# Performance work log

Measured on AMD Instinct MI355X. Metric: run time of the kernel, lower is better.

## Reference

```python
import jax, jax.numpy as jnp
import numpy as np

T, H, I, E, K = 1024, 2880, 2880, 16, 4
ALPHA = 1.702   # gemm1_alpha
LIMIT = 7.0     # swiglu_limit (gemm1_clamp_limit)


def setup_inputs() -> dict:
    key = jax.random.key(0)
    ks = jax.random.split(key, 9)
    s = 0.02  # init scale to keep activations sane
    return {
        "hidden_states": jax.random.normal(ks[0], (T, H), jnp.float32),
        "router_w": jax.random.normal(ks[1], (E, H), jnp.float32) * s,
        "router_b": jax.random.normal(ks[2], (E,), jnp.float32) * s,
        "w_gate": jax.random.normal(ks[3], (E, H, I), jnp.float32) * s,
        "b_gate": jax.random.normal(ks[4], (E, I), jnp.float32) * s,
        "w_up": jax.random.normal(ks[5], (E, H, I), jnp.float32) * s,
        "b_up": jax.random.normal(ks[6], (E, I), jnp.float32) * s,
        "w_down": jax.random.normal(ks[7], (E, I, H), jnp.float32) * s,
        "b_down": jax.random.normal(ks[8], (E, H), jnp.float32) * s,
    }


def reference(hidden_states, router_w, router_b, w_gate, b_gate, w_up, b_up, w_down, b_down):
    x = hidden_states  # [T, H]
    # Router: ReplicatedLinear(hidden_size, num_experts, bias=True)
    logits = x @ router_w.T + router_b            # [T, E]
    # TopK(top_k=K, renormalize=True): softmax -> top-k -> renormalize
    probs = jax.nn.softmax(logits, axis=-1)
    top_w, top_i = jax.lax.top_k(probs, K)        # [T, K]
    top_w = top_w / jnp.sum(top_w, axis=-1, keepdims=True)
    # combine weights scattered back to [T, E] (rows sum to 1)
    comb = jnp.sum(jax.nn.one_hot(top_i, E, dtype=x.dtype) * top_w[..., None], axis=1)
    # Expert grouped GEMM (dense over experts; combine weights zero out unused)
    g = jnp.einsum('th,ehi->eti', x, w_gate) + b_gate[:, None, :]   # [E, T, I]
    u = jnp.einsum('th,ehi->eti', x, w_up) + b_up[:, None, :]       # [E, T, I]
    # gpt-oss clamped swiglu: gate clamp max, up clamp both sides
    g = jnp.minimum(g, LIMIT)
    u = jnp.clip(u, -LIMIT, LIMIT)
    act = (u + 1.0) * (g * jax.nn.sigmoid(g * ALPHA))               # [E, T, I]
    y = jnp.einsum('eti,eih->eth', act, w_down) + b_down[:, None, :]  # [E, T, H]
    out = jnp.einsum('te,eth->th', comb, y)                          # [T, H]
    return out
```

## Files before the change

### kernel.cpp

```cpp
#include <hip/hip_runtime.h>
#include <stdint.h>

#define T_TOK 1024
#define HD 2880
#define ID 2880
#define NE 16
#define NTOP 4

#define BM 128
#define BN 64
#define BK 64
#define NKT (HD / BK)
#define NIB (ID / BN)
#define NMB (T_TOK / BM)
#define NBLK (NE * NIB * NMB)

typedef short bf16x8 __attribute__((ext_vector_type(8)));
typedef float f32x4 __attribute__((ext_vector_type(4)));

__device__ __forceinline__ uint4 pack8f(const float* v) {
    union { __bf16 b[8]; uint4 q; } p;
#pragma unroll
    for (int j = 0; j < 8; j++) p.b[j] = (__bf16)v[j];
    return p.q;
}
__device__ __forceinline__ unsigned short bf16bits(float f) {
    union { __bf16 b[2]; unsigned short u[2]; } p;
    p.b[0] = (__bf16)f;
    return p.u[0];
}

__global__ __launch_bounds__(256) void k_init(float* __restrict__ out, int* __restrict__ cnt) {
    int i = blockIdx.x * 256 + threadIdx.x;
    ((float4*)out)[i] = make_float4(0.f, 0.f, 0.f, 0.f);
    if (blockIdx.x == 0 && threadIdx.x < NE) cnt[threadIdx.x] = 0;
}

__global__ __launch_bounds__(256) void k_xbf(const float* __restrict__ x, unsigned short* __restrict__ xbf) {
    const size_t i = (size_t)blockIdx.x * 256 + threadIdx.x;
    float v[8];
    float4 a = ((const float4*)x)[i * 2];
    float4 b = ((const float4*)x)[i * 2 + 1];
    v[0] = a.x; v[1] = a.y; v[2] = a.z; v[3] = a.w;
    v[4] = b.x; v[5] = b.y; v[6] = b.z; v[7] = b.w;
    ((uint4*)xbf)[i] = pack8f(v);
}

__global__ __launch_bounds__(256) void k_router(
    const float* __restrict__ x, const float* __restrict__ rw, const float* __restrict__ rb,
    float* __restrict__ topw, int* __restrict__ cnt, int* __restrict__ list)
{
    const int t = blockIdx.x;
    const int tid = threadIdx.x;
    float acc[NE];
#pragma unroll
    for (int e = 0; e < NE; e++) acc[e] = 0.f;
    for (int c = tid; c < HD; c += 256) {
        float xv = x[(size_t)t * HD + c];
#pragma unroll
        for (int e = 0; e < NE; e++) acc[e] += xv * rw[(size_t)e * HD + c];
    }
    __shared__ float red[4][NE];
    const int lane = tid & 63, wv = tid >> 6;
#pragma unroll
    for (int e = 0; e < NE; e++) {
        float v = acc[e];
#pragma unroll
        for (int off = 32; off > 0; off >>= 1) v += __shfl_down(v, off, 64);
        if (lane == 0) red[wv][e] = v;
    }
    __syncthreads();
    if (tid == 0) {
        float p[NE];
        float mx = -1e30f;
        for (int e = 0; e < NE; e++) {
            float v = red[0][e] + red[1][e] + red[2][e] + red[3][e] + rb[e];
            p[e] = v; mx = fmaxf(mx, v);
        }
        for (int e = 0; e < NE; e++) p[e] = expf(p[e] - mx);
        int sel[NTOP]; float pw[NTOP]; float ssum = 0.f;
        for (int k = 0; k < NTOP; k++) {
            float best = -1.f; int bi = 0;
            for (int e = 0; e < NE; e++)
                if (p[e] > best) { best = p[e]; bi = e; }
            sel[k] = bi; pw[k] = best; ssum += best; p[bi] = -2.f;
        }
        for (int k = 0; k < NTOP; k++) {
            topw[t * NTOP + k] = pw[k] / ssum;
            int e = sel[k];
            int pos = atomicAdd(&cnt[e], 1);
            list[e * T_TOK + pos] = t * NTOP + k;
        }
    }
}

__global__ void k_scan(const int* __restrict__ cnt, int* __restrict__ offs) {
    if (threadIdx.x == 0 && blockIdx.x == 0) {
        int s = 0;
        for (int e = 0; e < NE; e++) { offs[e] = s; s += cnt[e]; }
        offs[NE] = s;
    }
}

__global__ __launch_bounds__(512) void k_gemm1(
    const unsigned short* __restrict__ xbf,
    const float* __restrict__ wg, const float* __restrict__ bg,
    const float* __restrict__ wu, const float* __restrict__ bu,
    const int* __restrict__ cnt, const int* __restrict__ offs,
    const int* __restrict__ list,
    unsigned short* __restrict__ act)
{
    const int lin = blockIdx.x;
    const int logical = (lin & 7) * (NBLK / 8) + (lin >> 3);
    const int mblk = logical & 7;
    const int iblk = (logical >> 3) % NIB;
    const int e = logical / (NIB * NMB);

    const int count = cnt[e];
    const int m0 = mblk * BM;
    if (m0 >= count) return;
    const int mcount = min(BM, count - m0);
    const int i0 = iblk * BN;
    const int tid = threadIdx.x;

    __shared__ char sA[BM * BK * 2];
    __shared__ char sG[BN * BK * 2];
    __shared__ char sU[BN * BK * 2];
    __shared__ int lidx[BM];

    if (tid < BM) lidx[tid] = list[e * T_TOK + m0 + min(tid, mcount - 1)];
    __syncthreads();

    const int lane = tid & 63, wid = tid >> 6;
    const int wm = wid >> 1, wn = wid & 1;
    const int lr = lane & 15, lk = lane >> 4;

    const int arw0 = wid * 8 + (lane >> 3);
    const int arw1 = 64 + arw0;
    const int asl = ((lane & 7) ^ ((lane >> 3) & 7)) * 8;
    const unsigned short* ga0 = xbf + (size_t)(lidx[arw0] >> 2) * HD + asl;
    const unsigned short* ga1 = xbf + (size_t)(lidx[arw1] >> 2) * HD + asl;
    char* const lb0 = sA + (wid * 8) * 128;
    char* const lb1 = sA + (64 + wid * 8) * 128;

    const int wtid = tid & 255;
    const int wc = wtid & 63, whg = wtid >> 6;
    const float* wsrc = (tid < 256 ? wg : wu) + ((size_t)e * HD + whg * 16) * ID + i0 + wc;
    char* const wdst = (tid < 256 ? sG : sU);

    f32x4 accG[2][2], accU[2][2];
#pragma unroll
    for (int mb = 0; mb < 2; mb++)
#pragma unroll
        for (int cb = 0; cb < 2; cb++) {
            accG[mb][cb] = (f32x4){0.f, 0.f, 0.f, 0.f};
            accU[mb][cb] = (f32x4){0.f, 0.f, 0.f, 0.f};
        }

    for (int kt = 0; kt < NKT; kt++) {
        __builtin_amdgcn_global_load_lds(ga0 + kt * BK, lb0, 16, 0, 0);
        __builtin_amdgcn_global_load_lds(ga1 + kt * BK, lb1, 16, 0, 0);
        {
            float v[16];
#pragma unroll
            for (int j = 0; j < 16; j++) v[j] = wsrc[(size_t)(kt * BK + j) * ID];
            *(uint4*)(wdst + wc * 128 + (((whg * 2) ^ (wc & 7)) * 16)) = pack8f(v);
            *(uint4*)(wdst + wc * 128 + (((whg * 2 + 1) ^ (wc & 7)) * 16)) = pack8f(v + 8);
        }
        __syncthreads();
#pragma unroll
        for (int ks = 0; ks < 2; ks++) {
            const int s = ks * 4 + lk;
            bf16x8 af[2], gf[2], uf[2];
#pragma unroll
            for (int mb = 0; mb < 2; mb++) {
                int rr = wm * 32 + mb * 16 + lr;
                af[mb] = *(const bf16x8*)(sA + rr * 128 + ((s ^ (rr & 7)) * 16));
            }
#pragma unroll
            for (int cb = 0; cb < 2; cb++) {
                int ii = wn * 32 + cb * 16 + lr;
                gf[cb] = *(const bf16x8*)(sG + ii * 128 + ((s ^ (ii & 7)) * 16));
                uf[cb] = *(const bf16x8*)(sU + ii * 128 + ((s ^ (ii & 7)) * 16));
            }
#pragma unroll
            for (int mb = 0; mb < 2; mb++)
#pragma unroll
                for (int cb = 0; cb < 2; cb++) {
                    accG[mb][cb] = __builtin_amdgcn_mfma_f32_16x16x32_bf16(af[mb], gf[cb], accG[mb][cb], 0, 0, 0);
                    accU[mb][cb] = __builtin_amdgcn_mfma_f32_16x16x32_bf16(af[mb], uf[cb], accU[mb][cb], 0, 0, 0);
                }
        }
        __syncthreads();
    }

    const int gbase = offs[e] + m0;
#pragma unroll
    for (int mb = 0; mb < 2; mb++)
#pragma unroll
        for (int cb = 0; cb < 2; cb++) {
            const int col = i0 + wn * 32 + cb * 16 + lr;
            const float bgv = bg[e * ID + col];
            const float buv = bu[e * ID + col];
#pragma unroll
            for (int q = 0; q < 4; q++) {
                const int r = wm * 32 + mb * 16 + lk * 4 + q;
                if (r < mcount) {
                    float gv = fminf(accG[mb][cb][q] + bgv, 7.0f);
                    float uv = fminf(fmaxf(accU[mb][cb][q] + buv, -7.0f), 7.0f);
                    float av = (uv + 1.0f) * (gv / (1.0f + __expf(-1.702f * gv)));
                    act[(size_t)(gbase + r) * ID + col] = bf16bits(av);
                }
            }
        }
}

__global__ __launch_bounds__(512) void k_gemm2(
    const unsigned short* __restrict__ act,
    const float* __restrict__ wd, const float* __restrict__ bd,
    const float* __restrict__ topw,
    const int* __restrict__ cnt, const int* __restrict__ offs,
    const int* __restrict__ list,
    float* __restrict__ out)
{
    const int lin = blockIdx.x;
    const int logical = (lin & 7) * (NBLK / 8) + (lin >> 3);
    const int mblk = logical & 7;
    const int hblk = (logical >> 3) % NIB;
    const int e = logical / (NIB * NMB);

    const int count = cnt[e];
    const int m0 = mblk * BM;
    if (m0 >= count) return;
    const int mcount = min(BM, count - m0);
    const int h0 = hblk * BN;
    const int tid = threadIdx.x;
    const int gbase = offs[e] + m0;

    __shared__ char sA[BM * BK * 2];
    __shared__ char sW[BN * BK * 2];
    __shared__ int lidx[BM];

    if (tid < BM) lidx[tid] = list[e * T_TOK + m0 + min(tid, mcount - 1)];
    __syncthreads();

    const int lane = tid & 63, wid = tid >> 6;
    const int wm = wid >> 1, wn = wid & 1;
    const int lr = lane & 15, lk = lane >> 4;

    const int arw0 = wid * 8 + (lane >> 3);
    const int arw1 = 64 + arw0;
    const int asl = ((lane & 7) ^ ((lane >> 3) & 7)) * 8;
    const unsigned short* ga0 = act + (size_t)(gbase + min(arw0, mcount - 1)) * ID + asl;
    const unsigned short* ga1 = act + (size_t)(gbase + min(arw1, mcount - 1)) * ID + asl;
    char* const lb0 = sA + (wid * 8) * 128;
    char* const lb1 = sA + (64 + wid * 8) * 128;

    const int wc = tid & 63, whg = tid >> 6;
    const float* wsrc = wd + (size_t)e * ID * HD + (size_t)(whg * 8) * HD + h0 + wc;

    f32x4 acc[2][2];
#pragma unroll
    for (int mb = 0; mb < 2; mb++)
#pragma unroll
        for (int cb = 0; cb < 2; cb++) acc[mb][cb] = (f32x4){0.f, 0.f, 0.f, 0.f};

    for (int kt = 0; kt < NKT; kt++) {
        __builtin_amdgcn_global_load_lds(ga0 + kt * BK, lb0, 16, 0, 0);
        __builtin_amdgcn_global_load_lds(ga1 + kt * BK, lb1, 16, 0, 0);
        {
            float v[8];
#pragma unroll
            for (int j = 0; j < 8; j++) v[j] = wsrc[(size_t)(kt * BK + j) * HD];
            *(uint4*)(sW + wc * 128 + ((whg ^ (wc & 7)) * 16)) = pack8f(v);
        }
        __syncthreads();
#pragma unroll
        for (int ks = 0; ks < 2; ks++) {
            const int s = ks * 4 + lk;
            bf16x8 af[2], wf[2];
#pragma unroll
            for (int mb = 0; mb < 2; mb++) {
                int rr = wm * 32 + mb * 16 + lr;
                af[mb] = *(const bf16x8*)(sA + rr * 128 + ((s ^ (rr & 7)) * 16));
            }
#pragma unroll
            for (int cb = 0; cb < 2; cb++) {
                int ii = wn * 32 + cb * 16 + lr;
                wf[cb] = *(const bf16x8*)(sW + ii * 128 + ((s ^ (ii & 7)) * 16));
            }
#pragma unroll
            for (int mb = 0; mb < 2; mb++)
#pragma unroll
                for (int cb = 0; cb < 2; cb++)
                    acc[mb][cb] = __builtin_amdgcn_mfma_f32_16x16x32_bf16(af[mb], wf[cb], acc[mb][cb], 0, 0, 0);
        }
        __syncthreads();
    }

#pragma unroll
    for (int mb = 0; mb < 2; mb++)
#pragma unroll
        for (int cb = 0; cb < 2; cb++) {
            const int col = h0 + wn * 32 + cb * 16 + lr;
            const float bdv = bd[e * HD + col];
#pragma unroll
            for (int q = 0; q < 4; q++) {
                const int r = wm * 32 + mb * 16 + lk * 4 + q;
                if (r < mcount) {
                    int idx = lidx[r];
                    float w = topw[idx];
                    atomicAdd(&out[(size_t)(idx >> 2) * HD + col], w * (acc[mb][cb][q] + bdv));
                }
            }
        }
}

extern "C" void kernel_launch(void* const* d_in, const int* in_sizes, int n_in,
                              void* d_out, int out_size, void* d_ws, size_t ws_size,
                              hipStream_t stream)
{
    const float* x  = (const float*)d_in[0];
    const float* rw = (const float*)d_in[1];
    const float* rb = (const float*)d_in[2];
    const float* wg = (const float*)d_in[3];
    const float* bg = (const float*)d_in[4];
    const float* wu = (const float*)d_in[5];
    const float* bu = (const float*)d_in[6];
    const float* wd = (const float*)d_in[7];
    const float* bd = (const float*)d_in[8];
    float* out = (float*)d_out;

    char* ws = (char*)d_ws;
    int*   cnt  = (int*)(ws + 0);
    int*   offs = (int*)(ws + 256);
    float* topw = (float*)(ws + 1024);
    int*   list = (int*)(ws + 32768);
    unsigned short* act = (unsigned short*)(ws + 131072);
    unsigned short* xbf = (unsigned short*)(ws + 131072 + (size_t)4096 * ID * 2);

    hipLaunchKernelGGL(k_init, dim3(T_TOK * HD / 1024), dim3(256), 0, stream, out, cnt);
    hipLaunchKernelGGL(k_xbf, dim3(T_TOK * HD / (256 * 8)), dim3(256), 0, stream, x, xbf);
    hipLaunchKernelGGL(k_router, dim3(T_TOK), dim3(256), 0, stream, x, rw, rb, topw, cnt, list);
    hipLaunchKernelGGL(k_scan, dim3(1), dim3(64), 0, stream, cnt, offs);
    hipLaunchKernelGGL(k_gemm1, dim3(NBLK), dim3(512), 0, stream,
                       xbf, wg, bg, wu, bu, cnt, offs, list, act);
    hipLaunchKernelGGL(k_gemm2, dim3(NBLK), dim3(512), 0, stream,
                       act, wd, bd, topw, cnt, offs, list, out);
}
```

Measured before the change: 1.094 ms.

## Double-buffer weight tiles, load A from global into registers, enlarge gemm2 M tile

Both expert GEMMs now keep the fp32-to-bf16 weight tile in a double-buffered LDS ring. The next tile's global loads are issued before the MFMAs and the LDS store comes after them, so only one barrier remains per K step. Activation (A) fragments are read straight from global memory into registers instead of being staged through LDS. In gemm1 each warp now computes both gate and up tiles, and the SwiGLU is combined through an LDS exchange. gemm2 uses a 256-row M tile so each weight tile is reused across more tokens, at the cost of more registers, uncoalesced direct A loads, and fewer blocks.

Measured after the change: 2.342 ms. 114% more time.

```diff
diff --git a/kernel.cpp b/kernel.cpp
--- a/kernel.cpp
+++ b/kernel.cpp
@@ -6,14 +6,20 @@
 #define ID 2880
 #define NE 16
 #define NTOP 4
-
-#define BM 128
-#define BN 64
 #define BK 64
 #define NKT (HD / BK)
-#define NIB (ID / BN)
-#define NMB (T_TOK / BM)
-#define NBLK (NE * NIB * NMB)
+
+#define G1_BM 128
+#define G1_BN 64
+#define G1_NIB (ID / G1_BN)
+#define G1_NMB (T_TOK / G1_BM)
+#define G1_NB (NE * G1_NIB * G1_NMB)
+
+#define G2_BM 256
+#define G2_BN 64
+#define G2_NHB (HD / G2_BN)
+#define G2_NMB (T_TOK / G2_BM)
+#define G2_NB (NE * G2_NHB * G2_NMB)
 
 typedef short bf16x8 __attribute__((ext_vector_type(8)));
 typedef float f32x4 __attribute__((ext_vector_type(4)));
@@ -102,7 +108,7 @@
     }
 }
 
-__global__ __launch_bounds__(512) void k_gemm1(
+__global__ __launch_bounds__(512, 4) void k_gemm1(
     const unsigned short* __restrict__ xbf,
     const float* __restrict__ wg, const float* __restrict__ bg,
     const float* __restrict__ wu, const float* __restrict__ bu,
@@ -111,111 +117,129 @@
     unsigned short* __restrict__ act)
 {
     const int lin = blockIdx.x;
-    const int logical = (lin & 7) * (NBLK / 8) + (lin >> 3);
+    const int logical = (lin & 7) * (G1_NB / 8) + (lin >> 3);
     const int mblk = logical & 7;
-    const int iblk = (logical >> 3) % NIB;
-    const int e = logical / (NIB * NMB);
+    const int iblk = (logical >> 3) % G1_NIB;
+    const int e = logical / (G1_NIB * G1_NMB);
 
     const int count = cnt[e];
-    const int m0 = mblk * BM;
+    const int m0 = mblk * G1_BM;
     if (m0 >= count) return;
-    const int mcount = min(BM, count - m0);
-    const int i0 = iblk * BN;
+    const int mcount = min(G1_BM, count - m0);
+    const int i0 = iblk * G1_BN;
     const int tid = threadIdx.x;
 
-    __shared__ char sA[BM * BK * 2];
-    __shared__ char sG[BN * BK * 2];
-    __shared__ char sU[BN * BK * 2];
-    __shared__ int lidx[BM];
-
-    if (tid < BM) lidx[tid] = list[e * T_TOK + m0 + min(tid, mcount - 1)];
+    __shared__ __align__(16) char sW[2][2][8192];
+    __shared__ float sgl[128][66];
+    __shared__ int lidx[G1_BM];
+
+    if (tid < G1_BM) lidx[tid] = list[e * T_TOK + m0 + min(tid, mcount - 1)];
     __syncthreads();
 
     const int lane = tid & 63, wid = tid >> 6;
-    const int wm = wid >> 1, wn = wid & 1;
+    const int wm = wid >> 2;
+    const int wn = (wid >> 1) & 1;
+    const int mg = wid & 1;
     const int lr = lane & 15, lk = lane >> 4;
 
-    const int arw0 = wid * 8 + (lane >> 3);
-    const int arw1 = 64 + arw0;
-    const int asl = ((lane & 7) ^ ((lane >> 3) & 7)) * 8;
-    const unsigned short* ga0 = xbf + (size_t)(lidx[arw0] >> 2) * HD + asl;
-    const unsigned short* ga1 = xbf + (size_t)(lidx[arw1] >> 2) * HD + asl;
-    char* const lb0 = sA + (wid * 8) * 128;
-    char* const lb1 = sA + (64 + wid * 8) * 128;
+    const unsigned short* arow[4];
+#pragma unroll
+    for (int mb = 0; mb < 4; mb++)
+        arow[mb] = xbf + (size_t)(lidx[wm * 64 + mb * 16 + lr] >> 2) * HD;
 
     const int wtid = tid & 255;
     const int wc = wtid & 63, whg = wtid >> 6;
     const float* wsrc = (tid < 256 ? wg : wu) + ((size_t)e * HD + whg * 16) * ID + i0 + wc;
-    char* const wdst = (tid < 256 ? sG : sU);
-
-    f32x4 accG[2][2], accU[2][2];
-#pragma unroll
-    for (int mb = 0; mb < 2; mb++)
+    const int wmat = tid >> 8;
+
+    f32x4 acc[4][2];
+#pragma unroll
+    for (int mb = 0; mb < 4; mb++)
+#pragma unroll
+        for (int cb = 0; cb < 2; cb++) acc[mb][cb] = (f32x4){0.f, 0.f, 0.f, 0.f};
+
+    float wv[16];
+    {
+#pragma unroll
+        for (int j = 0; j < 16; j++) wv[j] = wsrc[(size_t)j * ID];
+        char* wd = &sW[0][wmat][0];
+        *(uint4*)(wd + wc * 128 + (((whg * 2) ^ (wc & 7)) * 16)) = pack8f(wv);
+        *(uint4*)(wd + wc * 128 + (((whg * 2 + 1) ^ (wc & 7)) * 16)) = pack8f(wv + 8);
+    }
+    __syncthreads();
+
+    for (int kt = 0; kt < NKT; kt++) {
+        const bool more = (kt + 1 < NKT);
+        bf16x8 af[4][2];
+#pragma unroll
+        for (int mb = 0; mb < 4; mb++)
+#pragma unroll
+            for (int ks = 0; ks < 2; ks++)
+                af[mb][ks] = *(const bf16x8*)(arow[mb] + kt * BK + (ks * 4 + lk) * 8);
+        if (more) {
+#pragma unroll
+            for (int j = 0; j < 16; j++) wv[j] = wsrc[(size_t)((kt + 1) * BK + j) * ID];
+        }
+        __builtin_amdgcn_sched_barrier(0);
+        const char* base = &sW[kt & 1][0][0];
 #pragma unroll
         for (int cb = 0; cb < 2; cb++) {
-            accG[mb][cb] = (f32x4){0.f, 0.f, 0.f, 0.f};
-            accU[mb][cb] = (f32x4){0.f, 0.f, 0.f, 0.f};
-        }
-
-    for (int kt = 0; kt < NKT; kt++) {
-        __builtin_amdgcn_global_load_lds(ga0 + kt * BK, lb0, 16, 0, 0);
-        __builtin_amdgcn_global_load_lds(ga1 + kt * BK, lb1, 16, 0, 0);
-        {
-            float v[16];
-#pragma unroll
-            for (int j = 0; j < 16; j++) v[j] = wsrc[(size_t)(kt * BK + j) * ID];
-            *(uint4*)(wdst + wc * 128 + (((whg * 2) ^ (wc & 7)) * 16)) = pack8f(v);
-            *(uint4*)(wdst + wc * 128 + (((whg * 2 + 1) ^ (wc & 7)) * 16)) = pack8f(v + 8);
+            const char* mbase = base + ((cb ^ mg) ? 8192 : 0);
+            const int ii = wn * 32 + cb * 16 + lr;
+#pragma unroll
+            for (int ks = 0; ks < 2; ks++) {
+                const int s = ks * 4 + lk;
+                bf16x8 bf = *(const bf16x8*)(mbase + ii * 128 + ((s ^ (ii & 7)) * 16));
+#pragma unroll
+                for (int mb = 0; mb < 4; mb++)
+                    acc[mb][cb] = __builtin_amdgcn_mfma_f32_16x16x32_bf16(af[mb][ks], bf, acc[mb][cb], 0, 0, 0);
+            }
+        }
+        if (more) {
+            char* wd = &sW[(kt + 1) & 1][wmat][0];
+            *(uint4*)(wd + wc * 128 + (((whg * 2) ^ (wc & 7)) * 16)) = pack8f(wv);
+            *(uint4*)(wd + wc * 128 + (((whg * 2 + 1) ^ (wc & 7)) * 16)) = pack8f(wv + 8);
         }
         __syncthreads();
-#pragma unroll
-        for (int ks = 0; ks < 2; ks++) {
-            const int s = ks * 4 + lk;
-            bf16x8 af[2], gf[2], uf[2];
-#pragma unroll
-            for (int mb = 0; mb < 2; mb++) {
-                int rr = wm * 32 + mb * 16 + lr;
-                af[mb] = *(const bf16x8*)(sA + rr * 128 + ((s ^ (rr & 7)) * 16));
-            }
-#pragma unroll
-            for (int cb = 0; cb < 2; cb++) {
-                int ii = wn * 32 + cb * 16 + lr;
-                gf[cb] = *(const bf16x8*)(sG + ii * 128 + ((s ^ (ii & 7)) * 16));
-                uf[cb] = *(const bf16x8*)(sU + ii * 128 + ((s ^ (ii & 7)) * 16));
-            }
-#pragma unroll
-            for (int mb = 0; mb < 2; mb++)
-#pragma unroll
-                for (int cb = 0; cb < 2; cb++) {
-                    accG[mb][cb] = __builtin_amdgcn_mfma_f32_16x16x32_bf16(af[mb], gf[cb], accG[mb][cb], 0, 0, 0);
-                    accU[mb][cb] = __builtin_amdgcn_mfma_f32_16x16x32_bf16(af[mb], uf[cb], accU[mb][cb], 0, 0, 0);
+    }
+
+    const int gbase = offs[e] + m0;
+#pragma unroll
+    for (int cb = 0; cb < 2; cb++) {
+        if (cb == mg) {
+            const int colg = wn * 32 + cb * 16 + lr;
+            const float bgv = bg[e * ID + i0 + colg];
+#pragma unroll
+            for (int mb = 0; mb < 4; mb++)
+#pragma unroll
+                for (int q = 0; q < 4; q++) {
+                    const int row = wm * 64 + mb * 16 + lk * 4 + q;
+                    float gv = fminf(acc[mb][cb][q] + bgv, 7.0f);
+                    sgl[row][colg] = gv / (1.0f + __expf(-1.702f * gv));
                 }
         }
-        __syncthreads();
-    }
-
-    const int gbase = offs[e] + m0;
-#pragma unroll
-    for (int mb = 0; mb < 2; mb++)
-#pragma unroll
-        for (int cb = 0; cb < 2; cb++) {
-            const int col = i0 + wn * 32 + cb * 16 + lr;
-            const float bgv = bg[e * ID + col];
-            const float buv = bu[e * ID + col];
-#pragma unroll
-            for (int q = 0; q < 4; q++) {
-                const int r = wm * 32 + mb * 16 + lk * 4 + q;
-                if (r < mcount) {
-                    float gv = fminf(accG[mb][cb][q] + bgv, 7.0f);
-                    float uv = fminf(fmaxf(accU[mb][cb][q] + buv, -7.0f), 7.0f);
-                    float av = (uv + 1.0f) * (gv / (1.0f + __expf(-1.702f * gv)));
-                    act[(size_t)(gbase + r) * ID + col] = bf16bits(av);
+    }
+    __syncthreads();
+#pragma unroll
+    for (int cb = 0; cb < 2; cb++) {
+        if (cb != mg) {
+            const int colu = wn * 32 + cb * 16 + lr;
+            const float buv = bu[e * ID + i0 + colu];
+#pragma unroll
+            for (int mb = 0; mb < 4; mb++)
+#pragma unroll
+                for (int q = 0; q < 4; q++) {
+                    const int row = wm * 64 + mb * 16 + lk * 4 + q;
+                    if (row < mcount) {
+                        float uv = fminf(fmaxf(acc[mb][cb][q] + buv, -7.0f), 7.0f) + 1.0f;
+                        act[(size_t)(gbase + row) * ID + i0 + colu] = bf16bits(uv * sgl[row][colu]);
+                    }
                 }
-            }
-        }
-}
-
-__global__ __launch_bounds__(512) void k_gemm2(
+        }
+    }
+}
+
+__global__ __launch_bounds__(512, 4) void k_gemm2(
     const unsigned short* __restrict__ act,
     const float* __restrict__ wd, const float* __restrict__ bd,
     const float* __restrict__ topw,
@@ -224,89 +248,92 @@
     float* __restrict__ out)
 {
     const int lin = blockIdx.x;
-    const int logical = (lin & 7) * (NBLK / 8) + (lin >> 3);
-    const int mblk = logical & 7;
-    const int hblk = (logical >> 3) % NIB;
-    const int e = logical / (NIB * NMB);
+    const int logical = (lin & 7) * (G2_NB / 8) + (lin >> 3);
+    const int mblk = logical & 3;
+    const int hblk = (logical >> 2) % G2_NHB;
+    const int e = logical / (G2_NHB * G2_NMB);
 
     const int count = cnt[e];
-    const int m0 = mblk * BM;
+    const int m0 = mblk * G2_BM;
     if (m0 >= count) return;
-    const int mcount = min(BM, count - m0);
-    const int h0 = hblk * BN;
+    const int mcount = min(G2_BM, count - m0);
+    const int h0 = hblk * G2_BN;
     const int tid = threadIdx.x;
     const int gbase = offs[e] + m0;
 
-    __shared__ char sA[BM * BK * 2];
-    __shared__ char sW[BN * BK * 2];
-    __shared__ int lidx[BM];
-
-    if (tid < BM) lidx[tid] = list[e * T_TOK + m0 + min(tid, mcount - 1)];
+    __shared__ __align__(16) char sW[2][8192];
+    __shared__ int lidx[G2_BM];
+
+    if (tid < G2_BM) lidx[tid] = list[e * T_TOK + m0 + min(tid, mcount - 1)];
     __syncthreads();
 
     const int lane = tid & 63, wid = tid >> 6;
     const int wm = wid >> 1, wn = wid & 1;
     const int lr = lane & 15, lk = lane >> 4;
 
-    const int arw0 = wid * 8 + (lane >> 3);
-    const int arw1 = 64 + arw0;
-    const int asl = ((lane & 7) ^ ((lane >> 3) & 7)) * 8;
-    const unsigned short* ga0 = act + (size_t)(gbase + min(arw0, mcount - 1)) * ID + asl;
-    const unsigned short* ga1 = act + (size_t)(gbase + min(arw1, mcount - 1)) * ID + asl;
-    char* const lb0 = sA + (wid * 8) * 128;
-    char* const lb1 = sA + (64 + wid * 8) * 128;
+    const unsigned short* arow[4];
+#pragma unroll
+    for (int mb = 0; mb < 4; mb++)
+        arow[mb] = act + (size_t)(gbase + min(wm * 64 + mb * 16 + lr, mcount - 1)) * ID;
 
     const int wc = tid & 63, whg = tid >> 6;
-    const float* wsrc = wd + (size_t)e * ID * HD + (size_t)(whg * 8) * HD + h0 + wc;
-
-    f32x4 acc[2][2];
-#pragma unroll
-    for (int mb = 0; mb < 2; mb++)
+    const float* wsrc = wd + (size_t)e * (size_t)ID * HD + (size_t)(whg * 8) * HD + h0 + wc;
+
+    f32x4 acc[4][2];
+#pragma unroll
+    for (int mb = 0; mb < 4; mb++)
 #pragma unroll
         for (int cb = 0; cb < 2; cb++) acc[mb][cb] = (f32x4){0.f, 0.f, 0.f, 0.f};
 
+    float wv[8];
+    {
+#pragma unroll
+        for (int j = 0; j < 8; j++) wv[j] = wsrc[(size_t)j * HD];
+        *(uint4*)(sW[0] + wc * 128 + ((whg ^ (wc & 7)) * 16)) = pack8f(wv);
+    }
+    __syncthreads();
+
     for (int kt = 0; kt < NKT; kt++) {
-        __builtin_amdgcn_global_load_lds(ga0 + kt * BK, lb0, 16, 0, 0);
-        __builtin_amdgcn_global_load_lds(ga1 + kt * BK, lb1, 16, 0, 0);
-        {
-            float v[8];
-#pragma unroll
-            for (int j = 0; j < 8; j++) v[j] = wsrc[(size_t)(kt * BK + j) * HD];
-            *(uint4*)(sW + wc * 128 + ((whg ^ (wc & 7)) * 16)) = pack8f(v);
+        const bool more = (kt + 1 < NKT);
+        bf16x8 af[4][2];
+#pragma unroll
+        for (int mb = 0; mb < 4; mb++)
+#pragma unroll
+            for (int ks = 0; ks < 2; ks++)
+                af[mb][ks] = *(const bf16x8*)(arow[mb] + kt * BK + (ks * 4 + lk) * 8);
+        if (more) {
+#pragma unroll
+            for (int j = 0; j < 8; j++) wv[j] = wsrc[(size_t)((kt + 1) * BK + j) * HD];
+        }
+        __builtin_amdgcn_sched_barrier(0);
+        const char* base = sW[kt & 1];
+#pragma unroll
+        for (int cb = 0; cb < 2; cb++) {
+            const int ii = wn * 32 + cb * 16 + lr;
+#pragma unroll
+            for (int ks = 0; ks < 2; ks++) {
+                const int s = ks * 4 + lk;
+                bf16x8 bf = *(const bf16x8*)(base + ii * 128 + ((s ^ (ii & 7)) * 16));
+#pragma unroll
+                for (int mb = 0; mb < 4; mb++)
+                    acc[mb][cb] = __builtin_amdgcn_mfma_f32_16x16x32_bf16(af[mb][ks], bf, acc[mb][cb], 0, 0, 0);
+            }
+        }
+        if (more) {
+            *(uint4*)(sW[(kt + 1) & 1] + wc * 128 + ((whg ^ (wc & 7)) * 16)) = pack8f(wv);
         }
         __syncthreads();
-#pragma unroll
-        for (int ks = 0; ks < 2; ks++) {
-            const int s = ks * 4 + lk;
-            bf16x8 af[2], wf[2];
-#pragma unroll
-            for (int mb = 0; mb < 2; mb++) {
-                int rr = wm * 32 + mb * 16 + lr;
-                af[mb] = *(const bf16x8*)(sA + rr * 128 + ((s ^ (rr & 7)) * 16));
-            }
-#pragma unroll
-            for (int cb = 0; cb < 2; cb++) {
-                int ii = wn * 32 + cb * 16 + lr;
-                wf[cb] = *(const bf16x8*)(sW + ii * 128 + ((s ^ (ii & 7)) * 16));
-            }
-#pragma unroll
-            for (int mb = 0; mb < 2; mb++)
-#pragma unroll
-                for (int cb = 0; cb < 2; cb++)
-                    acc[mb][cb] = __builtin_amdgcn_mfma_f32_16x16x32_bf16(af[mb], wf[cb], acc[mb][cb], 0, 0, 0);
-        }
-        __syncthreads();
-    }
-
-#pragma unroll
-    for (int mb = 0; mb < 2; mb++)
+    }
+
+#pragma unroll
+    for (int mb = 0; mb < 4; mb++)
 #pragma unroll
         for (int cb = 0; cb < 2; cb++) {
             const int col = h0 + wn * 32 + cb * 16 + lr;
             const float bdv = bd[e * HD + col];
 #pragma unroll
             for (int q = 0; q < 4; q++) {
-                const int r = wm * 32 + mb * 16 + lk * 4 + q;
+                const int r = wm * 64 + mb * 16 + lk * 4 + q;
                 if (r < mcount) {
                     int idx = lidx[r];
                     float w = topw[idx];
@@ -343,8 +370,8 @@
     hipLaunchKernelGGL(k_xbf, dim3(T_TOK * HD / (256 * 8)), dim3(256), 0, stream, x, xbf);
     hipLaunchKernelGGL(k_router, dim3(T_TOK), dim3(256), 0, stream, x, rw, rb, topw, cnt, list);
     hipLaunchKernelGGL(k_scan, dim3(1), dim3(64), 0, stream, cnt, offs);
-    hipLaunchKernelGGL(k_gemm1, dim3(NBLK), dim3(512), 0, stream,
+    hipLaunchKernelGGL(k_gemm1, dim3(G1_NB), dim3(512), 0, stream,
                        xbf, wg, bg, wu, bu, cnt, offs, list, act);
-    hipLaunchKernelGGL(k_gemm2, dim3(NBLK), dim3(512), 0, stream,
+    hipLaunchKernelGGL(k_gemm2, dim3(G2_NB), dim3(512), 0, stream,
                        act, wd, bd, topw, cnt, offs, list, out);
 }
```

## Split GEMM blocks into producer/consumer warps with double-buffered weight tiles

Applied to the files above, without the earlier changes.

Both expert GEMM kernels now dedicate four warps to loading and converting fp32 weight tiles into a double-buffered LDS area, while the other four warps run the MFMAs. The consumer warps read activation rows straight from global memory into registers instead of staging them in LDS, and each consumer covers a 64x32 output tile. Priority hints are raised around the MFMA section and launch bounds ask for more occupancy. The aim is to overlap the strided fp32 weight loads with compute. The cost is that only half the warps do math, A fragments now come from scattered uncached global reads, and register pressure rises.

Result: slower. 1.507 ms (+37.8%).

```diff
diff --git a/kernel.cpp b/kernel.cpp
--- a/kernel.cpp
+++ b/kernel.cpp
@@ -6,11 +6,11 @@
 #define ID 2880
 #define NE 16
 #define NTOP 4
+#define BK 64
+#define NKT (HD / BK)
 
 #define BM 128
 #define BN 64
-#define BK 64
-#define NKT (HD / BK)
 #define NIB (ID / BN)
 #define NMB (T_TOK / BM)
 #define NBLK (NE * NIB * NMB)
@@ -102,7 +102,7 @@
     }
 }
 
-__global__ __launch_bounds__(512) void k_gemm1(
+__global__ __launch_bounds__(512, 4) void k_gemm1(
     const unsigned short* __restrict__ xbf,
     const float* __restrict__ wg, const float* __restrict__ bg,
     const float* __restrict__ wu, const float* __restrict__ bu,
@@ -123,99 +123,120 @@
     const int i0 = iblk * BN;
     const int tid = threadIdx.x;
 
-    __shared__ char sA[BM * BK * 2];
-    __shared__ char sG[BN * BK * 2];
-    __shared__ char sU[BN * BK * 2];
+    __shared__ __align__(16) char sGU[2][2][BN * BK * 2];
     __shared__ int lidx[BM];
 
     if (tid < BM) lidx[tid] = list[e * T_TOK + m0 + min(tid, mcount - 1)];
     __syncthreads();
 
     const int lane = tid & 63, wid = tid >> 6;
-    const int wm = wid >> 1, wn = wid & 1;
+    const bool producer = (wid >= 4);
+
+    const int ptid = tid & 255;
+    const int wc = ptid & 63, sel = ptid >> 6;
+    const int mat = sel & 1, kh = sel >> 1;
+    const float* wsrc = (mat ? wu : wg) + ((size_t)e * HD + kh * 32) * ID + i0 + wc;
+    char* const pdst0 = &sGU[0][mat][0] + wc * 128;
+    char* const pdst1 = &sGU[1][mat][0] + wc * 128;
+
+    const int mh = wid >> 1, nh = wid & 1;
     const int lr = lane & 15, lk = lane >> 4;
-
-    const int arw0 = wid * 8 + (lane >> 3);
-    const int arw1 = 64 + arw0;
-    const int asl = ((lane & 7) ^ ((lane >> 3) & 7)) * 8;
-    const unsigned short* ga0 = xbf + (size_t)(lidx[arw0] >> 2) * HD + asl;
-    const unsigned short* ga1 = xbf + (size_t)(lidx[arw1] >> 2) * HD + asl;
-    char* const lb0 = sA + (wid * 8) * 128;
-    char* const lb1 = sA + (64 + wid * 8) * 128;
-
-    const int wtid = tid & 255;
-    const int wc = wtid & 63, whg = wtid >> 6;
-    const float* wsrc = (tid < 256 ? wg : wu) + ((size_t)e * HD + whg * 16) * ID + i0 + wc;
-    char* const wdst = (tid < 256 ? sG : sU);
-
-    f32x4 accG[2][2], accU[2][2];
-#pragma unroll
-    for (int mb = 0; mb < 2; mb++)
+    const unsigned short* arow[4];
+#pragma unroll
+    for (int mb = 0; mb < 4; mb++)
+        arow[mb] = xbf + (size_t)(lidx[mh * 64 + mb * 16 + lr] >> 2) * HD;
+
+    f32x4 accG[4][2], accU[4][2];
+#pragma unroll
+    for (int mb = 0; mb < 4; mb++)
 #pragma unroll
         for (int cb = 0; cb < 2; cb++) {
             accG[mb][cb] = (f32x4){0.f, 0.f, 0.f, 0.f};
             accU[mb][cb] = (f32x4){0.f, 0.f, 0.f, 0.f};
         }
 
+    if (producer) {
+        float v[32];
+#pragma unroll
+        for (int j = 0; j < 32; j++) v[j] = wsrc[(size_t)j * ID];
+#pragma unroll
+        for (int jj = 0; jj < 4; jj++) {
+            const int s = kh * 4 + jj;
+            *(uint4*)(pdst0 + ((s ^ (wc & 7)) * 16)) = pack8f(v + jj * 8);
+        }
+    }
+    __syncthreads();
+
     for (int kt = 0; kt < NKT; kt++) {
-        __builtin_amdgcn_global_load_lds(ga0 + kt * BK, lb0, 16, 0, 0);
-        __builtin_amdgcn_global_load_lds(ga1 + kt * BK, lb1, 16, 0, 0);
-        {
-            float v[16];
-#pragma unroll
-            for (int j = 0; j < 16; j++) v[j] = wsrc[(size_t)(kt * BK + j) * ID];
-            *(uint4*)(wdst + wc * 128 + (((whg * 2) ^ (wc & 7)) * 16)) = pack8f(v);
-            *(uint4*)(wdst + wc * 128 + (((whg * 2 + 1) ^ (wc & 7)) * 16)) = pack8f(v + 8);
+        if (producer) {
+            if (kt + 1 < NKT) {
+                const float* ws = wsrc + (size_t)(kt + 1) * BK * ID;
+                float v[32];
+#pragma unroll
+                for (int j = 0; j < 32; j++) v[j] = ws[(size_t)j * ID];
+                char* d = (kt & 1) ? pdst0 : pdst1;
+#pragma unroll
+                for (int jj = 0; jj < 4; jj++) {
+                    const int s = kh * 4 + jj;
+                    *(uint4*)(d + ((s ^ (wc & 7)) * 16)) = pack8f(v + jj * 8);
+                }
+            }
+        } else {
+            bf16x8 af[4][2];
+#pragma unroll
+            for (int mb = 0; mb < 4; mb++)
+#pragma unroll
+                for (int ks = 0; ks < 2; ks++)
+                    af[mb][ks] = *(const bf16x8*)(arow[mb] + kt * BK + (ks * 4 + lk) * 8);
+            const char* bG = &sGU[kt & 1][0][0];
+            const char* bU = &sGU[kt & 1][1][0];
+            __builtin_amdgcn_s_setprio(1);
+#pragma unroll
+            for (int ks = 0; ks < 2; ks++) {
+                const int s = ks * 4 + lk;
+#pragma unroll
+                for (int cb = 0; cb < 2; cb++) {
+                    const int ii = nh * 32 + cb * 16 + lr;
+                    const int off = ii * 128 + ((s ^ (ii & 7)) * 16);
+                    bf16x8 g = *(const bf16x8*)(bG + off);
+#pragma unroll
+                    for (int mb = 0; mb < 4; mb++)
+                        accG[mb][cb] = __builtin_amdgcn_mfma_f32_16x16x32_bf16(af[mb][ks], g, accG[mb][cb], 0, 0, 0);
+                    bf16x8 u = *(const bf16x8*)(bU + off);
+#pragma unroll
+                    for (int mb = 0; mb < 4; mb++)
+                        accU[mb][cb] = __builtin_amdgcn_mfma_f32_16x16x32_bf16(af[mb][ks], u, accU[mb][cb], 0, 0, 0);
+                }
+            }
+            __builtin_amdgcn_s_setprio(0);
         }
         __syncthreads();
-#pragma unroll
-        for (int ks = 0; ks < 2; ks++) {
-            const int s = ks * 4 + lk;
-            bf16x8 af[2], gf[2], uf[2];
-#pragma unroll
-            for (int mb = 0; mb < 2; mb++) {
-                int rr = wm * 32 + mb * 16 + lr;
-                af[mb] = *(const bf16x8*)(sA + rr * 128 + ((s ^ (rr & 7)) * 16));
-            }
-#pragma unroll
-            for (int cb = 0; cb < 2; cb++) {
-                int ii = wn * 32 + cb * 16 + lr;
-                gf[cb] = *(const bf16x8*)(sG + ii * 128 + ((s ^ (ii & 7)) * 16));
-                uf[cb] = *(const bf16x8*)(sU + ii * 128 + ((s ^ (ii & 7)) * 16));
-            }
-#pragma unroll
-            for (int mb = 0; mb < 2; mb++)
-#pragma unroll
-                for (int cb = 0; cb < 2; cb++) {
-                    accG[mb][cb] = __builtin_amdgcn_mfma_f32_16x16x32_bf16(af[mb], gf[cb], accG[mb][cb], 0, 0, 0);
-                    accU[mb][cb] = __builtin_amdgcn_mfma_f32_16x16x32_bf16(af[mb], uf[cb], accU[mb][cb], 0, 0, 0);
-                }
-        }
-        __syncthreads();
-    }
+    }
+
+    if (producer) return;
 
     const int gbase = offs[e] + m0;
 #pragma unroll
-    for (int mb = 0; mb < 2; mb++)
-#pragma unroll
-        for (int cb = 0; cb < 2; cb++) {
-            const int col = i0 + wn * 32 + cb * 16 + lr;
-            const float bgv = bg[e * ID + col];
-            const float buv = bu[e * ID + col];
+    for (int cb = 0; cb < 2; cb++) {
+        const int col = nh * 32 + cb * 16 + lr;
+        const float bgv = bg[e * ID + i0 + col];
+        const float buv = bu[e * ID + i0 + col];
+#pragma unroll
+        for (int mb = 0; mb < 4; mb++)
 #pragma unroll
             for (int q = 0; q < 4; q++) {
-                const int r = wm * 32 + mb * 16 + lk * 4 + q;
-                if (r < mcount) {
+                const int row = mh * 64 + mb * 16 + lk * 4 + q;
+                if (row < mcount) {
                     float gv = fminf(accG[mb][cb][q] + bgv, 7.0f);
                     float uv = fminf(fmaxf(accU[mb][cb][q] + buv, -7.0f), 7.0f);
                     float av = (uv + 1.0f) * (gv / (1.0f + __expf(-1.702f * gv)));
-                    act[(size_t)(gbase + r) * ID + col] = bf16bits(av);
-                }
-            }
-        }
-}
-
-__global__ __launch_bounds__(512) void k_gemm2(
+                    act[(size_t)(gbase + row) * ID + i0 + col] = bf16bits(av);
+                }
+            }
+    }
+}
+
+__global__ __launch_bounds__(512, 4) void k_gemm2(
     const unsigned short* __restrict__ act,
     const float* __restrict__ wd, const float* __restrict__ bd,
     const float* __restrict__ topw,
@@ -237,83 +258,104 @@
     const int tid = threadIdx.x;
     const int gbase = offs[e] + m0;
 
-    __shared__ char sA[BM * BK * 2];
-    __shared__ char sW[BN * BK * 2];
+    __shared__ __align__(16) char sW[2][BN * BK * 2];
     __shared__ int lidx[BM];
 
     if (tid < BM) lidx[tid] = list[e * T_TOK + m0 + min(tid, mcount - 1)];
     __syncthreads();
 
     const int lane = tid & 63, wid = tid >> 6;
-    const int wm = wid >> 1, wn = wid & 1;
+    const bool producer = (wid >= 4);
+
+    const int ptid = tid & 255;
+    const int wc = ptid & 63, kq = ptid >> 6;
+    const float* wsrc = wd + ((size_t)e * ID + kq * 16) * HD + h0 + wc;
+    char* const pdst0 = &sW[0][0] + wc * 128;
+    char* const pdst1 = &sW[1][0] + wc * 128;
+
+    const int mh = wid >> 1, nh = wid & 1;
     const int lr = lane & 15, lk = lane >> 4;
-
-    const int arw0 = wid * 8 + (lane >> 3);
-    const int arw1 = 64 + arw0;
-    const int asl = ((lane & 7) ^ ((lane >> 3) & 7)) * 8;
-    const unsigned short* ga0 = act + (size_t)(gbase + min(arw0, mcount - 1)) * ID + asl;
-    const unsigned short* ga1 = act + (size_t)(gbase + min(arw1, mcount - 1)) * ID + asl;
-    char* const lb0 = sA + (wid * 8) * 128;
-    char* const lb1 = sA + (64 + wid * 8) * 128;
-
-    const int wc = tid & 63, whg = tid >> 6;
-    const float* wsrc = wd + (size_t)e * ID * HD + (size_t)(whg * 8) * HD + h0 + wc;
-
-    f32x4 acc[2][2];
-#pragma unroll
-    for (int mb = 0; mb < 2; mb++)
+    const unsigned short* arow[4];
+#pragma unroll
+    for (int mb = 0; mb < 4; mb++)
+        arow[mb] = act + (size_t)(gbase + min(mh * 64 + mb * 16 + lr, mcount - 1)) * ID;
+
+    f32x4 acc[4][2];
+#pragma unroll
+    for (int mb = 0; mb < 4; mb++)
 #pragma unroll
         for (int cb = 0; cb < 2; cb++) acc[mb][cb] = (f32x4){0.f, 0.f, 0.f, 0.f};
 
+    if (producer) {
+        float v[16];
+#pragma unroll
+        for (int j = 0; j < 16; j++) v[j] = wsrc[(size_t)j * HD];
+#pragma unroll
+        for (int jj = 0; jj < 2; jj++) {
+            const int s = kq * 2 + jj;
+            *(uint4*)(pdst0 + ((s ^ (wc & 7)) * 16)) = pack8f(v + jj * 8);
+        }
+    }
+    __syncthreads();
+
     for (int kt = 0; kt < NKT; kt++) {
-        __builtin_amdgcn_global_load_lds(ga0 + kt * BK, lb0, 16, 0, 0);
-        __builtin_amdgcn_global_load_lds(ga1 + kt * BK, lb1, 16, 0, 0);
-        {
-            float v[8];
-#pragma unroll
-            for (int j = 0; j < 8; j++) v[j] = wsrc[(size_t)(kt * BK + j) * HD];
-            *(uint4*)(sW + wc * 128 + ((whg ^ (wc & 7)) * 16)) = pack8f(v);
+        if (producer) {
+            if (kt + 1 < NKT) {
+                const float* ws = wsrc + (size_t)(kt + 1) * BK * HD;
+                float v[16];
+#pragma unroll
+                for (int j = 0; j < 16; j++) v[j] = ws[(size_t)j * HD];
+                char* d = (kt & 1) ? pdst0 : pdst1;
+#pragma unroll
+                for (int jj = 0; jj < 2; jj++) {
+                    const int s = kq * 2 + jj;
+                    *(uint4*)(d + ((s ^ (wc & 7)) * 16)) = pack8f(v + jj * 8);
+                }
+            }
+        } else {
+            bf16x8 af[4][2];
+#pragma unroll
+            for (int mb = 0; mb < 4; mb++)
+#pragma unroll
+                for (int ks = 0; ks < 2; ks++)
+                    af[mb][ks] = *(const bf16x8*)(arow[mb] + kt * BK + (ks * 4 + lk) * 8);
+            const char* bW = &sW[kt & 1][0];
+            __builtin_amdgcn_s_setprio(1);
+#pragma unroll
+            for (int ks = 0; ks < 2; ks++) {
+                const int s = ks * 4 + lk;
+#pragma unroll
+                for (int cb = 0; cb < 2; cb++) {
+                    const int ii = nh * 32 + cb * 16 + lr;
+                    bf16x8 w = *(const bf16x8*)(bW + ii * 128 + ((s ^ (ii & 7)) * 16));
+#pragma unroll
+                    for (int mb = 0; mb < 4; mb++)
+                        acc[mb][cb] = __builtin_amdgcn_mfma_f32_16x16x32_bf16(af[mb][ks], w, acc[mb][cb], 0, 0, 0);
+                }
+            }
+            __builtin_amdgcn_s_setprio(0);
         }
         __syncthreads();
-#pragma unroll
-        for (int ks = 0; ks < 2; ks++) {
-            const int s = ks * 4 + lk;
-            bf16x8 af[2], wf[2];
-#pragma unroll
-            for (int mb = 0; mb < 2; mb++) {
-                int rr = wm * 32 + mb * 16 + lr;
-                af[mb] = *(const bf16x8*)(sA + rr * 128 + ((s ^ (rr & 7)) * 16));
-            }
-#pragma unroll
-            for (int cb = 0; cb < 2; cb++) {
-                int ii = wn * 32 + cb * 16 + lr;
-                wf[cb] = *(const bf16x8*)(sW + ii * 128 + ((s ^ (ii & 7)) * 16));
-            }
-#pragma unroll
-            for (int mb = 0; mb < 2; mb++)
-#pragma unroll
-                for (int cb = 0; cb < 2; cb++)
-                    acc[mb][cb] = __builtin_amdgcn_mfma_f32_16x16x32_bf16(af[mb], wf[cb], acc[mb][cb], 0, 0, 0);
-        }
-        __syncthreads();
-    }
-
-#pragma unroll
-    for (int mb = 0; mb < 2; mb++)
-#pragma unroll
-        for (int cb = 0; cb < 2; cb++) {
-            const int col = h0 + wn * 32 + cb * 16 + lr;
-            const float bdv = bd[e * HD + col];
+    }
+
+    if (producer) return;
+
+#pragma unroll
+    for (int cb = 0; cb < 2; cb++) {
+        const int col = h0 + nh * 32 + cb * 16 + lr;
+        const float bdv = bd[e * HD + col];
+#pragma unroll
+        for (int mb = 0; mb < 4; mb++)
 #pragma unroll
             for (int q = 0; q < 4; q++) {
-                const int r = wm * 32 + mb * 16 + lk * 4 + q;
+                const int r = mh * 64 + mb * 16 + lk * 4 + q;
                 if (r < mcount) {
-                    int idx = lidx[r];
-                    float w = topw[idx];
+                    const int idx = lidx[r];
+                    const float w = topw[idx];
                     atomicAdd(&out[(size_t)(idx >> 2) * HD + col], w * (acc[mb][cb][q] + bdv));
                 }
             }
-        }
+    }
 }
 
 extern "C" void kernel_launch(void* const* d_in, const int* in_sizes, int n_in,
```
